# Performance work log

Hardware: AMD Instinct MI355X
Metric: run time of the kernel (lower is better)

The kernel has to match this reference:

```python
import itertools
import jax, jax.numpy as jnp
import numpy as np

LATENT_DIM = 16
POLY_ORDER = 2
STATE_DIM = 16
BATCH, T = 64, 8192

# Precompute sklearn PolynomialFeatures term index lists (include_bias=True ordering):
# degree 0 (bias), degree 1 (x_i), degree 2 (combinations_with_replacement lexicographic), ...
_DEG_TERMS = []  # list (per degree>=2) of np arrays of shape (n_terms, degree)
for d in range(2, POLY_ORDER + 1):
    _DEG_TERMS.append(np.array(list(itertools.combinations_with_replacement(range(LATENT_DIM), d)), dtype=np.int32))
LIBRARY_DIM = 1 + LATENT_DIM + sum(t.shape[0] for t in _DEG_TERMS) + LATENT_DIM  # +sine


def _sindy_library(x):
    # x: (B, T, n). Returns Theta: (B, T, library_dim), sklearn ordering + sin(x) appended.
    feats = [jnp.ones(x.shape[:-1] + (1,), dtype=x.dtype), x]
    for terms in _DEG_TERMS:
        # product over the `degree` indexed columns for each term, vectorized
        prod = x[..., terms[:, 0]]
        for c in range(1, terms.shape[1]):
            prod = prod * x[..., terms[:, c]]
        feats.append(prod)
    feats.append(jnp.sin(x))
    return jnp.concatenate(feats, axis=-1)


def setup_inputs() -> dict:
    key = jax.random.key(0)
    k1, k2 = jax.random.split(key)
    x = jax.random.normal(k1, (BATCH, T, LATENT_DIM), dtype=jnp.float32)
    # xavier-uniform-ish init for coefficients
    limit = np.sqrt(6.0 / (LIBRARY_DIM + STATE_DIM)).astype(np.float32)
    sindy_coefficients = jax.random.uniform(k2, (LIBRARY_DIM, STATE_DIM), dtype=jnp.float32, minval=-limit, maxval=limit)
    coefficient_mask = jnp.ones((LIBRARY_DIM, STATE_DIM), dtype=jnp.float32)
    return {"x": x, "sindy_coefficients": sindy_coefficients, "coefficient_mask": coefficient_mask}


def reference(x, sindy_coefficients, coefficient_mask):
    theta = _sindy_library(x)  # (B, T, L)
    # masked coefficient matmul: x_dot = Theta @ (mask * Xi)
    return jnp.einsum('btl,ld->btd', theta, coefficient_mask * sindy_coefficients)
```

## Files before the change

kernel.cpp:

```cpp
#include <hip/hip_runtime.h>
#include <hip/hip_bf16.h>

#define LATENT 16
#define STATE  16
#define NPOS   (64 * 8192)
#define NTILES (NPOS / 16)

typedef __attribute__((ext_vector_type(4))) float f32x4;
typedef __attribute__((ext_vector_type(8))) short bf16x8;

static __device__ __forceinline__ short f2bf(float f) {
    __hip_bfloat16 h = __float2bfloat16(f);
    return (short)__builtin_bit_cast(unsigned short, h);
}

__global__ __launch_bounds__(256) void prep_pack(const float* __restrict__ coef,
                                                 const float* __restrict__ mask,
                                                 float* __restrict__ wsf) {
    int id = blockIdx.x * 256 + threadIdx.x;
    if (id < 16) wsf[id] = coef[id] * mask[id];
    if (id >= 4608) return;
    int jj  = id & 7;
    int col = (id >> 3) & 15;
    int g   = (id >> 7) & 3;
    int c   = id >> 9;
    int k   = c * 32 + g * 8 + jj;
    float scale = 1.0f;
    int row;
    if (k < 256) {
        int I = k >> 4, J = k & 15;
        int im = I < J ? I : J, jm = I < J ? J : I;
        int q = im * 16 - im * (im - 1) / 2 + (jm - im);
        row = 17 + q;
        if (I != J) scale = 0.5f;
    } else if (k < 272) {
        row = 1 + (k - 256);
    } else {
        row = 153 + (k - 272);
    }
    float w = coef[row * STATE + col] * mask[row * STATE + col] * scale;
    ((ushort*)(wsf + 16))[id] = (ushort)f2bf(w);
}

__global__ __launch_bounds__(256, 4) void sindy_mfma(const float* __restrict__ x,
                                                     const float* __restrict__ wsf,
                                                     float* __restrict__ out) {
    const int lane  = threadIdx.x & 63;
    const int wid   = threadIdx.x >> 6;
    const int g     = lane >> 4;
    const int col   = lane & 15;
    const bool hiJ  = (g & 1) != 0;
    const bool hiI  = (g >> 1) != 0;

    const int tile = blockIdx.x * 4 + wid;
    const long base = (long)(tile * 16 + col) * 4;

    const float4* x4 = (const float4*)x;
    const float4 A = x4[base + 0];
    const float4 B = x4[base + 1];
    const float4 C = x4[base + 2];
    const float4 D = x4[base + 3];

    const ushort* Wpack = (const ushort*)(wsf + 16);
    const bf16x8 b0 = *(const bf16x8*)(Wpack + (0 * 64 + lane) * 8);
    const bf16x8 b1 = *(const bf16x8*)(Wpack + (1 * 64 + lane) * 8);
    const bf16x8 b2 = *(const bf16x8*)(Wpack + (2 * 64 + lane) * 8);
    const bf16x8 b3 = *(const bf16x8*)(Wpack + (3 * 64 + lane) * 8);
    const bf16x8 b4 = *(const bf16x8*)(Wpack + (4 * 64 + lane) * 8);
    const bf16x8 b5 = *(const bf16x8*)(Wpack + (5 * 64 + lane) * 8);
    const bf16x8 b6 = *(const bf16x8*)(Wpack + (6 * 64 + lane) * 8);
    const bf16x8 b7 = *(const bf16x8*)(Wpack + (7 * 64 + lane) * 8);
    const bf16x8 b8 = *(const bf16x8*)(Wpack + (8 * 64 + lane) * 8);

    const float4 bias4 = *(const float4*)(wsf + g * 4);

    const float xv0 = hiJ ? C.x : A.x;
    const float xv1 = hiJ ? C.y : A.y;
    const float xv2 = hiJ ? C.z : A.z;
    const float xv3 = hiJ ? C.w : A.w;
    const float xv4 = hiJ ? D.x : B.x;
    const float xv5 = hiJ ? D.y : B.y;
    const float xv6 = hiJ ? D.z : B.z;
    const float xv7 = hiJ ? D.w : B.w;
    const float xi0 = hiI ? A.y : A.x;
    const float xi1 = hiI ? A.w : A.z;
    const float xi2 = hiI ? B.y : B.x;
    const float xi3 = hiI ? B.w : B.z;
    const float xi4 = hiI ? C.y : C.x;
    const float xi5 = hiI ? C.w : C.z;
    const float xi6 = hiI ? D.y : D.x;
    const float xi7 = hiI ? D.w : D.z;

    f32x4 acc = {bias4.x, bias4.y, bias4.z, bias4.w};

#define QUAD(BF, XI)                                                     \
    {                                                                    \
        bf16x8 af;                                                       \
        af[0] = f2bf((XI) * xv0); af[1] = f2bf((XI) * xv1);              \
        af[2] = f2bf((XI) * xv2); af[3] = f2bf((XI) * xv3);              \
        af[4] = f2bf((XI) * xv4); af[5] = f2bf((XI) * xv5);              \
        af[6] = f2bf((XI) * xv6); af[7] = f2bf((XI) * xv7);              \
        acc = __builtin_amdgcn_mfma_f32_16x16x32_bf16(BF, af, acc, 0, 0, 0); \
    }
    QUAD(b0, xi0) QUAD(b1, xi1) QUAD(b2, xi2) QUAD(b3, xi3)
    QUAD(b4, xi4) QUAD(b5, xi5) QUAD(b6, xi6) QUAD(b7, xi7)
#undef QUAD
    {
        const bool us = (g >= 2);
        bf16x8 af;
        af[0] = f2bf(us ? __sinf(xv0) : xv0);
        af[1] = f2bf(us ? __sinf(xv1) : xv1);
        af[2] = f2bf(us ? __sinf(xv2) : xv2);
        af[3] = f2bf(us ? __sinf(xv3) : xv3);
        af[4] = f2bf(us ? __sinf(xv4) : xv4);
        af[5] = f2bf(us ? __sinf(xv5) : xv5);
        af[6] = f2bf(us ? __sinf(xv6) : xv6);
        af[7] = f2bf(us ? __sinf(xv7) : xv7);
        acc = __builtin_amdgcn_mfma_f32_16x16x32_bf16(b8, af, acc, 0, 0, 0);
    }

    float4 res;
    res.x = acc[0]; res.y = acc[1]; res.z = acc[2]; res.w = acc[3];
    *(float4*)(out + (long)(tile * 16 + col) * STATE + g * 4) = res;
}

extern "C" void kernel_launch(void* const* d_in, const int* in_sizes, int n_in,
                              void* d_out, int out_size, void* d_ws, size_t ws_size,
                              hipStream_t stream) {
    const float* x    = (const float*)d_in[0];
    const float* coef = (const float*)d_in[1];
    const float* mask = (const float*)d_in[2];
    float*       wsf  = (float*)d_ws;
    float*       out  = (float*)d_out;

    prep_pack<<<18, 256, 0, stream>>>(coef, mask, wsf);
    sindy_mfma<<<NTILES / 4, 256, 0, stream>>>(x, wsf, out);
}
```

Before: 30.33 us.

## Stage packed weights in LDS and process multiple tiles per wave

Each block now copies the packed bf16 weight fragments into shared memory once and reads them from LDS per MFMA chunk. Each wave loops over several 16-row tiles instead of one, so the grid shrinks and the weight load is spread over more work. Launch bounds raise the occupancy target. The cost is a block-level barrier, LDS reads inside the loop, and fewer blocks, which could leave less parallelism to hide memory latency.

```diff
diff --git a/kernel.cpp b/kernel.cpp
--- a/kernel.cpp
+++ b/kernel.cpp
@@ -5,6 +5,7 @@
 #define STATE  16
 #define NPOS   (64 * 8192)
 #define NTILES (NPOS / 16)
+#define TPW    4
 
 typedef __attribute__((ext_vector_type(4))) float f32x4;
 typedef __attribute__((ext_vector_type(8))) short bf16x8;
@@ -42,9 +43,17 @@
     ((ushort*)(wsf + 16))[id] = (ushort)f2bf(w);
 }
 
-__global__ __launch_bounds__(256, 4) void sindy_mfma(const float* __restrict__ x,
+__global__ __launch_bounds__(256, 8) void sindy_mfma(const float* __restrict__ x,
                                                      const float* __restrict__ wsf,
                                                      float* __restrict__ out) {
+    __shared__ uint4 wlds[576];
+    {
+        const uint4* src = (const uint4*)((const ushort*)(wsf + 16));
+        for (int i = threadIdx.x; i < 576; i += 256) wlds[i] = src[i];
+    }
+    __syncthreads();
+    const ushort* wl = (const ushort*)wlds;
+
     const int lane  = threadIdx.x & 63;
     const int wid   = threadIdx.x >> 6;
     const int g     = lane >> 4;
@@ -52,76 +61,70 @@
     const bool hiJ  = (g & 1) != 0;
     const bool hiI  = (g >> 1) != 0;
 
-    const int tile = blockIdx.x * 4 + wid;
-    const long base = (long)(tile * 16 + col) * 4;
+    const float4 bias4 = *(const float4*)(wsf + g * 4);
 
     const float4* x4 = (const float4*)x;
-    const float4 A = x4[base + 0];
-    const float4 B = x4[base + 1];
-    const float4 C = x4[base + 2];
-    const float4 D = x4[base + 3];
+    const int tile0 = (blockIdx.x * 4 + wid) * TPW;
 
-    const ushort* Wpack = (const ushort*)(wsf + 16);
-    const bf16x8 b0 = *(const bf16x8*)(Wpack + (0 * 64 + lane) * 8);
-    const bf16x8 b1 = *(const bf16x8*)(Wpack + (1 * 64 + lane) * 8);
-    const bf16x8 b2 = *(const bf16x8*)(Wpack + (2 * 64 + lane) * 8);
-    const bf16x8 b3 = *(const bf16x8*)(Wpack + (3 * 64 + lane) * 8);
-    const bf16x8 b4 = *(const bf16x8*)(Wpack + (4 * 64 + lane) * 8);
-    const bf16x8 b5 = *(const bf16x8*)(Wpack + (5 * 64 + lane) * 8);
-    const bf16x8 b6 = *(const bf16x8*)(Wpack + (6 * 64 + lane) * 8);
-    const bf16x8 b7 = *(const bf16x8*)(Wpack + (7 * 64 + lane) * 8);
-    const bf16x8 b8 = *(const bf16x8*)(Wpack + (8 * 64 + lane) * 8);
+    for (int t = 0; t < TPW; ++t) {
+        const int tile = tile0 + t;
+        const long base = (long)(tile * 16 + col) * 4;
+        const float4 A = x4[base + 0];
+        const float4 B = x4[base + 1];
+        const float4 C = x4[base + 2];
+        const float4 D = x4[base + 3];
 
-    const float4 bias4 = *(const float4*)(wsf + g * 4);
+        const float xv0 = hiJ ? C.x : A.x;
+        const float xv1 = hiJ ? C.y : A.y;
+        const float xv2 = hiJ ? C.z : A.z;
+        const float xv3 = hiJ ? C.w : A.w;
+        const float xv4 = hiJ ? D.x : B.x;
+        const float xv5 = hiJ ? D.y : B.y;
+        const float xv6 = hiJ ? D.z : B.z;
+        const float xv7 = hiJ ? D.w : B.w;
+        const float xi0 = hiI ? A.y : A.x;
+        const float xi1 = hiI ? A.w : A.z;
+        const float xi2 = hiI ? B.y : B.x;
+        const float xi3 = hiI ? B.w : B.z;
+        const float xi4 = hiI ? C.y : C.x;
+        const float xi5 = hiI ? C.w : C.z;
+        const float xi6 = hiI ? D.y : D.x;
+        const float xi7 = hiI ? D.w : D.z;
 
-    const float xv0 = hiJ ? C.x : A.x;
-    const float xv1 = hiJ ? C.y : A.y;
-    const float xv2 = hiJ ? C.z : A.z;
-    const float xv3 = hiJ ? C.w : A.w;
-    const float xv4 = hiJ ? D.x : B.x;
-    const float xv5 = hiJ ? D.y : B.y;
-    const float xv6 = hiJ ? D.z : B.z;
-    const float xv7 = hiJ ? D.w : B.w;
-    const float xi0 = hiI ? A.y : A.x;
-    const float xi1 = hiI ? A.w : A.z;
-    const float xi2 = hiI ? B.y : B.x;
-    const float xi3 = hiI ? B.w : B.z;
-    const float xi4 = hiI ? C.y : C.x;
-    const float xi5 = hiI ? C.w : C.z;
-    const float xi6 = hiI ? D.y : D.x;
-    const float xi7 = hiI ? D.w : D.z;
+        f32x4 acc = {bias4.x, bias4.y, bias4.z, bias4.w};
 
-    f32x4 acc = {bias4.x, bias4.y, bias4.z, bias4.w};
+#define CHUNK(CC, XI)                                                    \
+        {                                                                \
+            const bf16x8 bf = *(const bf16x8*)(wl + (CC * 64 + lane) * 8); \
+            bf16x8 af;                                                   \
+            af[0] = f2bf((XI) * xv0); af[1] = f2bf((XI) * xv1);          \
+            af[2] = f2bf((XI) * xv2); af[3] = f2bf((XI) * xv3);          \
+            af[4] = f2bf((XI) * xv4); af[5] = f2bf((XI) * xv5);          \
+            af[6] = f2bf((XI) * xv6); af[7] = f2bf((XI) * xv7);          \
+            acc = __builtin_amdgcn_mfma_f32_16x16x32_bf16(bf, af, acc, 0, 0, 0); \
+        }
+        CHUNK(0, xi0) CHUNK(1, xi1) CHUNK(2, xi2) CHUNK(3, xi3)
+        CHUNK(4, xi4) CHUNK(5, xi5) CHUNK(6, xi6) CHUNK(7, xi7)
+#undef CHUNK
+        {
+            const bool us = (g >= 2);
+            const bf16x8 bf = *(const bf16x8*)(wl + (8 * 64 + lane) * 8);
+            bf16x8 af;
+            af[0] = f2bf(us ? __sinf(xv0) : xv0);
+            af[1] = f2bf(us ? __sinf(xv1) : xv1);
+            af[2] = f2bf(us ? __sinf(xv2) : xv2);
+            af[3] = f2bf(us ? __sinf(xv3) : xv3);
+            af[4] = f2bf(us ? __sinf(xv4) : xv4);
+            af[5] = f2bf(us ? __sinf(xv5) : xv5);
+            af[6] = f2bf(us ? __sinf(xv6) : xv6);
+            af[7] = f2bf(us ? __sinf(xv7) : xv7);
+            acc = __builtin_amdgcn_mfma_f32_16x16x32_bf16(bf, af, acc, 0, 0, 0);
+        }
 
-#define QUAD(BF, XI)                                                     \
-    {                                                                    \
-        bf16x8 af;                                                       \
-        af[0] = f2bf((XI) * xv0); af[1] = f2bf((XI) * xv1);              \
-        af[2] = f2bf((XI) * xv2); af[3] = f2bf((XI) * xv3);              \
-        af[4] = f2bf((XI) * xv4); af[5] = f2bf((XI) * xv5);              \
-        af[6] = f2bf((XI) * xv6); af[7] = f2bf((XI) * xv7);              \
-        acc = __builtin_amdgcn_mfma_f32_16x16x32_bf16(BF, af, acc, 0, 0, 0); \
+        float4 res;
+        res.x = acc[0]; res.y = acc[1]; res.z = acc[2]; res.w = acc[3];
+        *(float4*)(out + (long)(tile * 16 + col) * STATE + g * 4) = res;
     }
-    QUAD(b0, xi0) QUAD(b1, xi1) QUAD(b2, xi2) QUAD(b3, xi3)
-    QUAD(b4, xi4) QUAD(b5, xi5) QUAD(b6, xi6) QUAD(b7, xi7)
-#undef QUAD
-    {
-        const bool us = (g >= 2);
-        bf16x8 af;
-        af[0] = f2bf(us ? __sinf(xv0) : xv0);
-        af[1] = f2bf(us ? __sinf(xv1) : xv1);
-        af[2] = f2bf(us ? __sinf(xv2) : xv2);
-        af[3] = f2bf(us ? __sinf(xv3) : xv3);
-        af[4] = f2bf(us ? __sinf(xv4) : xv4);
-        af[5] = f2bf(us ? __sinf(xv5) : xv5);
-        af[6] = f2bf(us ? __sinf(xv6) : xv6);
-        af[7] = f2bf(us ? __sinf(xv7) : xv7);
-        acc = __builtin_amdgcn_mfma_f32_16x16x32_bf16(b8, af, acc, 0, 0, 0);
-    }
-
-    float4 res;
-    res.x = acc[0]; res.y = acc[1]; res.z = acc[2]; res.w = acc[3];
-    *(float4*)(out + (long)(tile * 16 + col) * STATE + g * 4) = res;
 }
 
 extern "C" void kernel_launch(void* const* d_in, const int* in_sizes, int n_in,
@@ -134,5 +137,5 @@
     float*       out  = (float*)d_out;
 
     prep_pack<<<18, 256, 0, stream>>>(coef, mask, wsf);
-    sindy_mfma<<<NTILES / 4, 256, 0, stream>>>(x, wsf, out);
+    sindy_mfma<<<NTILES / (4 * TPW), 256, 0, stream>>>(x, wsf, out);
 }
```

Measured after the change: 31.21 us. 2.9% more time.
